# Kernel tuning notes

Hardware: AMD Instinct MI355X
Metric: run time of the kernel (lower is better)

Reference implementation:

```python
import jax, jax.numpy as jnp
import numpy as np

N = 50000       # nodes
E = 400000      # edges (before self-loops)
IN_C = 128
HID = 32        # hidden_channels per head
HEADS = 8
OUT_C = 64
K = 16          # num_clusters
NEG_SLOPE = 0.2
EPS = 1e-16


def setup_inputs() -> dict:
    key = jax.random.key(0)
    ks = jax.random.split(key, 14)
    g = lambda k, sh, sc: (jax.random.normal(k, sh, jnp.float32) * sc)
    return {
        "x": jax.random.normal(ks[0], (N, IN_C), jnp.float32),
        "edge_index": jax.random.randint(ks[1], (2, E), 0, N, dtype=jnp.int32),
        # GAT layer 1: in -> HEADS*HID
        "W1": g(ks[2], (IN_C, HEADS * HID), 0.08),
        "att_src1": g(ks[3], (HEADS, HID), 0.1),
        "att_dst1": g(ks[4], (HEADS, HID), 0.1),
        "b1": jnp.zeros((HEADS * HID,), jnp.float32),
        # GAT layer 2: HEADS*HID -> OUT_C, heads=1, concat=False
        "W2": g(ks[5], (HEADS * HID, OUT_C), 0.06),
        "att_src2": g(ks[6], (1, OUT_C), 0.1),
        "att_dst2": g(ks[7], (1, OUT_C), 0.1),
        "b2": jnp.zeros((OUT_C,), jnp.float32),
        # MLP head: OUT_C -> 128 -> K
        "Wm1": g(ks[8], (OUT_C, 128), 0.1),
        "bm1": jnp.zeros((128,), jnp.float32),
        "Wm2": g(ks[9], (128, K), 0.1),
        "bm2": jnp.zeros((K,), jnp.float32),
    }


def _gat_layer(x, W, att_src, att_dst, bias, src, dst, heads, ch, concat):
    # x: [N, F_in] -> h: [N, H, C]
    h = (x @ W).reshape(N, heads, ch)
    a_src = jnp.einsum('nhc,hc->nh', h, att_src)   # [N, H]
    a_dst = jnp.einsum('nhc,hc->nh', h, att_dst)   # [N, H]
    e = jax.nn.leaky_relu(a_src[src] + a_dst[dst], NEG_SLOPE)  # [Etot, H]
    # segment softmax over destination node
    m = jax.ops.segment_max(e, dst, num_segments=N)            # [N, H]
    ex = jnp.exp(e - m[dst])
    den = jax.ops.segment_sum(ex, dst, num_segments=N)         # [N, H]
    alpha = ex / (den[dst] + EPS)                              # [Etot, H]
    out = jax.ops.segment_sum(alpha[:, :, None] * h[src], dst, num_segments=N)  # [N, H, C]
    out = out.reshape(N, heads * ch) if concat else out.mean(axis=1)
    return out + bias


def reference(x, edge_index, W1, att_src1, att_dst1, b1, W2, att_src2, att_dst2, b2, Wm1, bm1, Wm2, bm2):
    # PyG GATConv adds self-loops by default
    loop = jnp.arange(N, dtype=edge_index.dtype)
    src = jnp.concatenate([edge_index[0], loop])
    dst = jnp.concatenate([edge_index[1], loop])
    # dropout layers are identity in eval mode
    h = jax.nn.elu(_gat_layer(x, W1, att_src1, att_dst1, b1, src, dst, HEADS, HID, True))
    embeddings = _gat_layer(h, W2, att_src2, att_dst2, b2, src, dst, 1, OUT_C, False)
    logits = jax.nn.relu(embeddings @ Wm1 + bm1) @ Wm2 + bm2
    s = jax.nn.softmax(logits, axis=1)
    return (s, embeddings)
```

## Files before the change

### kernel.cpp

```cpp
#include <hip/hip_runtime.h>
#include <hip/hip_fp16.h>
#include <math.h>

#define NNODES 50000
#define NEDGES 400000
#define INC    128
#define HC1    256
#define NHEADS 8
#define OUTC   64
#define NK     16
#define NEG_SLOPE 0.2f
#define EPS_F  1e-16f

typedef unsigned short u16;
typedef __attribute__((ext_vector_type(8))) short bf16x8;
typedef __attribute__((ext_vector_type(4))) float f32x4;

__device__ __forceinline__ float lrelu(float x){ return x > 0.f ? x : NEG_SLOPE * x; }
__device__ __forceinline__ float eluf(float x){ return x > 0.f ? x : (__expf(x) - 1.f); }
__device__ __forceinline__ float bf2f(u16 v){ return __uint_as_float((unsigned)v << 16); }
__device__ __forceinline__ u16 f2bf(float f){
    unsigned u = __float_as_uint(f);
    unsigned r = (u + 0x7FFFu + ((u >> 16) & 1u)) >> 16;
    return (u16)r;
}
__device__ __forceinline__ short f2bf_s(float f){ return (short)f2bf(f); }
__device__ __forceinline__ u16 f2h(float f){ return __half_as_ushort(__float2half(f)); }
__device__ __forceinline__ float h2f(u16 v){ return __half2float(__ushort_as_half(v)); }

__device__ __forceinline__ void fmix_lo(float& acc, unsigned w, float a){
    asm("v_fma_mix_f32 %0, %1, %2, %0 op_sel:[0,0,0] op_sel_hi:[1,0,0]"
        : "+v"(acc) : "v"(w), "v"(a));
}
__device__ __forceinline__ void fmix_hi(float& acc, unsigned w, float a){
    asm("v_fma_mix_f32 %0, %1, %2, %0 op_sel:[1,0,0] op_sel_hi:[1,0,0]"
        : "+v"(acc) : "v"(w), "v"(a));
}
__device__ __forceinline__ void mac8(float* acc, uint4 w, float a){
    fmix_lo(acc[0], w.x, a); fmix_hi(acc[1], w.x, a);
    fmix_lo(acc[2], w.y, a); fmix_hi(acc[3], w.y, a);
    fmix_lo(acc[4], w.z, a); fmix_hi(acc[5], w.z, a);
    fmix_lo(acc[6], w.w, a); fmix_hi(acc[7], w.w, a);
}
__device__ __forceinline__ void mac4(float4& acc, uint2 w, float a){
    fmix_lo(acc.x, w.x, a); fmix_hi(acc.y, w.x, a);
    fmix_lo(acc.z, w.y, a); fmix_hi(acc.w, w.y, a);
}

#define EB 1563
#define TB 232
__global__ void count_deg_tw_k(const int* __restrict__ dst, int* __restrict__ deg,
                               const float* __restrict__ W1, u16* __restrict__ W1t,
                               const float* __restrict__ W2, u16* __restrict__ W2t,
                               const float* __restrict__ Wm1, u16* __restrict__ W1mt,
                               const float* __restrict__ Wm2, u16* __restrict__ W2mt){
    if (blockIdx.x < EB){
        int e = blockIdx.x * 256 + threadIdx.x;
        if (e < NEDGES) atomicAdd(&deg[dst[e]], 1);
    } else {
        int i = (blockIdx.x - EB) * 256 + threadIdx.x;
        if (i < 32768){
            int n = i >> 7, k = i & 127;
            W1t[i] = f2bf(W1[k * 256 + n]);
        } else if (i < 49152){
            int ii = i - 32768;
            int n = ii >> 8, k = ii & 255;
            W2t[ii] = f2bf(W2[k * 64 + n]);
        } else if (i < 57344){
            int ii = i - 49152;
            int hd = ii >> 6, e = ii & 63;
            W1mt[ii] = f2bf(Wm1[e * 128 + hd]);
        } else if (i < 59392){
            int ii = i - 57344;
            int k = ii >> 7, hd = ii & 127;
            W2mt[ii] = f2bf(Wm2[hd * NK + k]);
        }
    }
}

__global__ void blocksum_k(const int* __restrict__ deg, int* __restrict__ bsum){
    __shared__ int sm[4];
    int i = blockIdx.x * 256 + threadIdx.x;
    int v = (i < NNODES) ? deg[i] : 0;
    for (int off = 1; off < 64; off <<= 1) v += __shfl_xor(v, off);
    int lane = threadIdx.x & 63, wid = threadIdx.x >> 6;
    if (lane == 0) sm[wid] = v;
    __syncthreads();
    if (threadIdx.x == 0) bsum[blockIdx.x] = sm[0] + sm[1] + sm[2] + sm[3];
}

__global__ void scan_write_k(const int* __restrict__ deg, const int* __restrict__ bsum,
                             int* __restrict__ rowptr){
    __shared__ int sm[4];
    __shared__ int sadd;
    int tid = threadIdx.x;
    int pv = (tid < blockIdx.x) ? bsum[tid] : 0;
    for (int off = 1; off < 64; off <<= 1) pv += __shfl_xor(pv, off);
    int lane = tid & 63, wid = tid >> 6;
    if (lane == 0) sm[wid] = pv;
    __syncthreads();
    if (tid == 0) sadd = sm[0] + sm[1] + sm[2] + sm[3];
    __syncthreads();

    int i = blockIdx.x * 256 + tid;
    int v = (i < NNODES) ? deg[i] : 0;
    int sv = v;
    for (int off = 1; off < 64; off <<= 1){ int t = __shfl_up(sv, off); if (lane >= off) sv += t; }
    __shared__ int wsum[4];
    if (lane == 63) wsum[wid] = sv;
    __syncthreads();
    int add = sadd;
    for (int w = 0; w < wid; w++) add += wsum[w];
    sv += add;
    if (i < NNODES) rowptr[i + 1] = sv;
    if (i == 0) rowptr[0] = 0;
}

__global__ void fill_csr_k(const int* __restrict__ src, const int* __restrict__ dst,
                           const int* __restrict__ rowptr, int* __restrict__ fillc,
                           int* __restrict__ col){
    int e = blockIdx.x * 256 + threadIdx.x;
    if (e < NEDGES){
        int d = dst[e];
        int pos = atomicAdd(&fillc[d], 1);
        col[rowptr[d] + pos] = src[e];
    }
}

__global__ __launch_bounds__(256, 4) void l1_k(const float* __restrict__ x, const u16* __restrict__ W1t,
                     const float* __restrict__ att_s, const float* __restrict__ att_d,
                     u16* __restrict__ h1bh, float* __restrict__ as1h, float* __restrict__ ad1h){
    __shared__ u16 Bs[16384];
    int tid = threadIdx.x;
    int lane = tid & 63, wid = tid >> 6;
    int ln = lane & 15, quad = lane >> 4;
    int m0 = blockIdx.x * 64 + wid * 16;
    int nb = blockIdx.y * 128;
    int hb = blockIdx.y * 4;
    int arow = m0 + ln; if (arow >= NNODES) arow = NNODES - 1;

#pragma unroll
    for (int it = 0; it < 8; it++){
        int p = it * 256 + tid;
        int c = p >> 6, l = p & 63;
        int snt = c & 7, skt = c >> 3;
        int sln = l & 15, sq = l >> 4;
        uint4 v = *(const uint4*)(W1t + (size_t)(nb + snt * 16 + sln) * INC + skt * 32 + sq * 8);
        *(uint4*)(&Bs[p * 8]) = v;
    }

    bf16x8 a[4];
#pragma unroll
    for (int kt = 0; kt < 4; kt++){
        const float* ap = x + (size_t)arow * INC + kt * 32 + quad * 8;
        float4 v0 = *(const float4*)ap;
        float4 v1 = *(const float4*)(ap + 4);
        bf16x8 t;
        t[0] = f2bf_s(v0.x); t[1] = f2bf_s(v0.y); t[2] = f2bf_s(v0.z); t[3] = f2bf_s(v0.w);
        t[4] = f2bf_s(v1.x); t[5] = f2bf_s(v1.y); t[6] = f2bf_s(v1.z); t[7] = f2bf_s(v1.w);
        a[kt] = t;
    }

    __syncthreads();

    f32x4 acc[8];
#pragma unroll
    for (int nt = 0; nt < 8; nt++) acc[nt] = (f32x4){0.f, 0.f, 0.f, 0.f};

#pragma unroll
    for (int kt = 0; kt < 4; kt++){
#pragma unroll
        for (int nt = 0; nt < 8; nt++){
            bf16x8 b = *(const bf16x8*)(&Bs[(kt * 8 + nt) * 512 + lane * 8]);
            acc[nt] = __builtin_amdgcn_mfma_f32_16x16x32_bf16(a[kt], b, acc[nt], 0, 0, 0);
        }
    }

#pragma unroll
    for (int i = 0; i < 4; i++){
        int r = m0 + quad * 4 + i;
        if (r < NNODES){
#pragma unroll
            for (int nt = 0; nt < 8; nt++){
                int c  = nb + nt * 16 + ln;
                int hh = c >> 5, c5 = c & 31;
                h1bh[((size_t)hh * NNODES + r) * 32 + c5] = f2h(acc[nt][i]);
            }
        }
    }

#pragma unroll
    for (int i = 0; i < 4; i++){
        int r = m0 + quad * 4 + i;
        float ps_keep = 0.f, pd_keep = 0.f;
#pragma unroll
        for (int h = 0; h < 4; h++){
            float ps = acc[2 * h][i]     * att_s[nb + h * 32 + ln]
                     + acc[2 * h + 1][i] * att_s[nb + h * 32 + 16 + ln];
            float pd = acc[2 * h][i]     * att_d[nb + h * 32 + ln]
                     + acc[2 * h + 1][i] * att_d[nb + h * 32 + 16 + ln];
            ps += __shfl_xor(ps, 1); pd += __shfl_xor(pd, 1);
            ps += __shfl_xor(ps, 2); pd += __shfl_xor(pd, 2);
            ps += __shfl_xor(ps, 4); pd += __shfl_xor(pd, 4);
            ps += __shfl_xor(ps, 8); pd += __shfl_xor(pd, 8);
            if (ln == h){ ps_keep = ps; pd_keep = pd; }
        }
        if (ln < 4 && r < NNODES){
            as1h[(size_t)(hb + ln) * NNODES + r] = ps_keep;
            ad1h[(size_t)(hb + ln) * NNODES + r] = pd_keep;
        }
    }
}

__global__ __launch_bounds__(256, 4) void l2_k(const u16* __restrict__ hL1b, const u16* __restrict__ W2t,
                     const float* __restrict__ att_s, const float* __restrict__ att_d,
                     u16* __restrict__ h2b, float* __restrict__ as2, float* __restrict__ ad2){
    __shared__ u16 Bs[16384];
    int tid = threadIdx.x;
    int lane = tid & 63, wid = tid >> 6;
    int ln = lane & 15, quad = lane >> 4;
    int m0 = blockIdx.x * 64 + wid * 16;
    int arow = m0 + ln; if (arow >= NNODES) arow = NNODES - 1;

#pragma unroll
    for (int it = 0; it < 8; it++){
        int p = it * 256 + tid;
        int c = p >> 6, l = p & 63;
        int snt = c & 3, skt = c >> 2;
        int sln = l & 15, sq = l >> 4;
        uint4 v = *(const uint4*)(W2t + (size_t)(snt * 16 + sln) * HC1 + skt * 32 + sq * 8);
        *(uint4*)(&Bs[p * 8]) = v;
    }

    __syncthreads();

    f32x4 acc[4];
#pragma unroll
    for (int nt = 0; nt < 4; nt++) acc[nt] = (f32x4){0.f, 0.f, 0.f, 0.f};

#pragma unroll
    for (int kt = 0; kt < 8; kt++){
        bf16x8 a = *(const bf16x8*)(hL1b + ((size_t)kt * NNODES + arow) * 32 + quad * 8);
#pragma unroll
        for (int nt = 0; nt < 4; nt++){
            bf16x8 b = *(const bf16x8*)(&Bs[(kt * 4 + nt) * 512 + lane * 8]);
            acc[nt] = __builtin_amdgcn_mfma_f32_16x16x32_bf16(a, b, acc[nt], 0, 0, 0);
        }
    }

#pragma unroll
    for (int i = 0; i < 4; i++){
        int r = m0 + quad * 4 + i;
        if (r < NNODES){
#pragma unroll
            for (int nt = 0; nt < 4; nt++)
                h2b[(size_t)r * OUTC + nt * 16 + ln] = f2h(acc[nt][i]);
        }
        float ps = acc[0][i] * att_s[ln]      + acc[1][i] * att_s[16 + ln]
                 + acc[2][i] * att_s[32 + ln] + acc[3][i] * att_s[48 + ln];
        float pd = acc[0][i] * att_d[ln]      + acc[1][i] * att_d[16 + ln]
                 + acc[2][i] * att_d[32 + ln] + acc[3][i] * att_d[48 + ln];
        ps += __shfl_xor(ps, 1); pd += __shfl_xor(pd, 1);
        ps += __shfl_xor(ps, 2); pd += __shfl_xor(pd, 2);
        ps += __shfl_xor(ps, 4); pd += __shfl_xor(pd, 4);
        ps += __shfl_xor(ps, 8); pd += __shfl_xor(pd, 8);
        if (ln == 0 && r < NNODES){ as2[r] = ps; ad2[r] = pd; }
    }
}

__global__ void gat1_agg_k(const u16* __restrict__ h1bh, const float* __restrict__ as1h,
                           const float* __restrict__ ad1h, const int* __restrict__ rowptr,
                           const int* __restrict__ col, const float* __restrict__ b1,
                           u16* __restrict__ outb){
    int lane = threadIdx.x & 63, wid = threadIdx.x >> 6;
    int g = lane >> 3, t = lane & 7;
    int h = blockIdx.x & 7;
    int d = (blockIdx.x >> 3) * 32 + wid * 8 + g;
    bool valid = (d < NNODES);
    int dd = valid ? d : (NNODES - 1);
    int row0 = rowptr[dd];
    int deg  = rowptr[dd + 1] - row0;

    const float* ash = as1h + (size_t)h * NNODES;
    float adst = ad1h[(size_t)h * NNODES + dd];
    const u16* hb = h1bh + (size_t)h * NNODES * 32;

    int sv0 = (t < deg)     ? col[row0 + t]     : dd;
    int sv1 = (8 + t < deg) ? col[row0 + 8 + t] : dd;
    uint2 wself = *(const uint2*)(hb + (size_t)dd * 32 + t * 4);
    float ev0 = ash[sv0];
    float ev1 = ash[sv1];

    float a_self = __expf(lrelu(ash[dd] + adst));
    float x0 = (t < deg)     ? __expf(lrelu(ev0 + adst)) : 0.f;
    float x1 = (8 + t < deg) ? __expf(lrelu(ev1 + adst)) : 0.f;

    float4 acc = make_float4(0.f, 0.f, 0.f, 0.f);
    mac4(acc, wself, a_self);

    int gb = g * 8;
    if (deg > 0){
        int s_arr[4]; float a_arr[4]; uint2 w_arr[4];
#pragma unroll
        for (int j = 0; j < 4; j++){ s_arr[j] = __shfl(sv0, gb + j); a_arr[j] = __shfl(x0, gb + j); }
#pragma unroll
        for (int j = 0; j < 4; j++) w_arr[j] = *(const uint2*)(hb + (size_t)s_arr[j] * 32 + t * 4);
#pragma unroll
        for (int j = 0; j < 4; j++) mac4(acc, w_arr[j], a_arr[j]);
        if (deg > 4){
#pragma unroll
            for (int j = 0; j < 4; j++){ s_arr[j] = __shfl(sv0, gb + 4 + j); a_arr[j] = __shfl(x0, gb + 4 + j); }
#pragma unroll
            for (int j = 0; j < 4; j++) w_arr[j] = *(const uint2*)(hb + (size_t)s_arr[j] * 32 + t * 4);
#pragma unroll
            for (int j = 0; j < 4; j++) mac4(acc, w_arr[j], a_arr[j]);
        }
    }
    if (deg > 8){
        int s_arr[4]; float a_arr[4]; uint2 w_arr[4];
#pragma unroll
        for (int j = 0; j < 4; j++){ s_arr[j] = __shfl(sv1, gb + j); a_arr[j] = __shfl(x1, gb + j); }
#pragma unroll
        for (int j = 0; j < 4; j++) w_arr[j] = *(const uint2*)(hb + (size_t)s_arr[j] * 32 + t * 4);
#pragma unroll
        for (int j = 0; j < 4; j++) mac4(acc, w_arr[j], a_arr[j]);
        if (deg > 12){
#pragma unroll
            for (int j = 0; j < 4; j++){ s_arr[j] = __shfl(sv1, gb + 4 + j); a_arr[j] = __shfl(x1, gb + 4 + j); }
#pragma unroll
            for (int j = 0; j < 4; j++) w_arr[j] = *(const uint2*)(hb + (size_t)s_arr[j] * 32 + t * 4);
#pragma unroll
            for (int j = 0; j < 4; j++) mac4(acc, w_arr[j], a_arr[j]);
        }
    }
    float tsum = 0.f;
    if (deg > 16){
        for (int idx = 16; idx < deg; idx++){
            int s = col[row0 + idx];
            float a = __expf(lrelu(ash[s] + adst));
            tsum += a;
            uint2 w = *(const uint2*)(hb + (size_t)s * 32 + t * 4);
            mac4(acc, w, a);
        }
    }

    float part = x0 + x1;
    part += __shfl_xor(part, 1);
    part += __shfl_xor(part, 2);
    part += __shfl_xor(part, 4);
    float rden = 1.f / (part + a_self + tsum + EPS_F);

    if (valid){
        float4 bb = *(const float4*)(b1 + h * 32 + t * 4);
        uint2 o;
        o.x = (unsigned)f2bf(eluf(acc.x * rden + bb.x)) | ((unsigned)f2bf(eluf(acc.y * rden + bb.y)) << 16);
        o.y = (unsigned)f2bf(eluf(acc.z * rden + bb.z)) | ((unsigned)f2bf(eluf(acc.w * rden + bb.w)) << 16);
        *(uint2*)(outb + ((size_t)h * NNODES + d) * 32 + t * 4) = o;
    }
}

__global__ void gat2_agg_k(const u16* __restrict__ h2b, const float* __restrict__ as2,
                           const float* __restrict__ ad2, const int* __restrict__ rowptr,
                           const int* __restrict__ col, const float* __restrict__ b2,
                           float* __restrict__ emb){
    int lane = threadIdx.x & 63, wid = threadIdx.x >> 6;
    int d = blockIdx.x * 4 + wid;
    int row0 = rowptr[d];
    int deg  = rowptr[d + 1] - row0;

    float adst = ad2[d];
    float a_self = __expf(lrelu(as2[d] + adst));

    if (deg <= 64){
        int sv = (lane < deg) ? col[row0 + lane] : d;
        float e_raw = as2[sv];

        int q = lane >> 4, c4 = (lane & 15) * 4;
        uint2 wself = *(const uint2*)(h2b + (unsigned)d * OUTC + c4);
        uint2 wpre[4];
#pragma unroll
        for (int k = 0; k < 4; k++){
            int s = __shfl(sv, k * 4 + q);
            wpre[k] = *(const uint2*)(h2b + (unsigned)s * OUTC + c4);
        }

        float x = (lane < deg) ? __expf(lrelu(e_raw + adst)) : 0.f;

        float a0 = (q == 0) ? a_self : 0.f;
        float4 acc = make_float4(0.f, 0.f, 0.f, 0.f);
        mac4(acc, wself, a0);
        {
            float a_arr[4];
#pragma unroll
            for (int k = 0; k < 4; k++) a_arr[k] = __shfl(x, k * 4 + q);
#pragma unroll
            for (int k = 0; k < 4; k++) mac4(acc, wpre[k], a_arr[k]);
        }
        for (int it0 = 16; it0 < deg; it0 += 16){
            int s_arr[4]; float a_arr[4];
#pragma unroll
            for (int k = 0; k < 4; k++){
                int itc = min(it0 + k * 4 + q, 63);
                s_arr[k] = __shfl(sv, itc);
                a_arr[k] = __shfl(x, itc);
            }
            uint2 w_arr[4];
#pragma unroll
            for (int k = 0; k < 4; k++)
                w_arr[k] = *(const uint2*)(h2b + (unsigned)s_arr[k] * OUTC + c4);
#pragma unroll
            for (int k = 0; k < 4; k++) mac4(acc, w_arr[k], a_arr[k]);
        }
        acc.x += __shfl_xor(acc.x, 16); acc.y += __shfl_xor(acc.y, 16);
        acc.z += __shfl_xor(acc.z, 16); acc.w += __shfl_xor(acc.w, 16);
        acc.x += __shfl_xor(acc.x, 32); acc.y += __shfl_xor(acc.y, 32);
        acc.z += __shfl_xor(acc.z, 32); acc.w += __shfl_xor(acc.w, 32);
        float vsum = x;
        for (int m = 1; m < 64; m <<= 1) vsum += __shfl_xor(vsum, m);
        float rden = 1.f / (vsum + a_self + EPS_F);
        if (lane < 16){
            float4 bb = *(const float4*)(b2 + c4);
            float4 o = make_float4(acc.x * rden + bb.x, acc.y * rden + bb.y,
                                   acc.z * rden + bb.z, acc.w * rden + bb.w);
            *(float4*)(emb + (size_t)d * OUTC + c4) = o;
        }
    } else {
        float vsum = a_self;
        float acc = a_self * h2f(h2b[(unsigned)d * OUTC + lane]);
        for (int idx = 0; idx < deg; idx++){
            int s = col[row0 + idx];
            float a = __expf(lrelu(as2[s] + adst));
            vsum += a;
            acc += a * h2f(h2b[(unsigned)s * OUTC + lane]);
        }
        emb[(size_t)d * OUTC + lane] = acc * (1.f / (vsum + EPS_F)) + b2[lane];
    }
}

__global__ void mlp_mfma_k(const float* __restrict__ emb, const u16* __restrict__ W1mt,
                           const float* __restrict__ bm1, const u16* __restrict__ W2mt,
                           const float* __restrict__ bm2, float* __restrict__ sout){
    __shared__ u16 hid[4][16][136];
    int lane = threadIdx.x & 63, wid = threadIdx.x >> 6;
    int ln = lane & 15, quad = lane >> 4;
    int m0 = blockIdx.x * 64 + wid * 16;
    int arow = m0 + ln; if (arow >= NNODES) arow = NNODES - 1;

    bf16x8 a[2];
#pragma unroll
    for (int kt = 0; kt < 2; kt++){
        const float* ap = emb + (size_t)arow * OUTC + kt * 32 + quad * 8;
        float4 v0 = *(const float4*)ap;
        float4 v1 = *(const float4*)(ap + 4);
        bf16x8 t;
        t[0] = f2bf_s(v0.x); t[1] = f2bf_s(v0.y); t[2] = f2bf_s(v0.z); t[3] = f2bf_s(v0.w);
        t[4] = f2bf_s(v1.x); t[5] = f2bf_s(v1.y); t[6] = f2bf_s(v1.z); t[7] = f2bf_s(v1.w);
        a[kt] = t;
    }

    f32x4 acc[8];
#pragma unroll
    for (int nt = 0; nt < 8; nt++) acc[nt] = (f32x4){0.f, 0.f, 0.f, 0.f};
#pragma unroll
    for (int kt = 0; kt < 2; kt++){
#pragma unroll
        for (int nt = 0; nt < 8; nt++){
            bf16x8 b = *(const bf16x8*)(W1mt + (size_t)(nt * 16 + ln) * OUTC + kt * 32 + quad * 8);
            acc[nt] = __builtin_amdgcn_mfma_f32_16x16x32_bf16(a[kt], b, acc[nt], 0, 0, 0);
        }
    }

#pragma unroll
    for (int nt = 0; nt < 8; nt++){
        float bb = bm1[nt * 16 + ln];
#pragma unroll
        for (int i = 0; i < 4; i++){
            float h = fmaxf(acc[nt][i] + bb, 0.f);
            hid[wid][quad * 4 + i][nt * 16 + ln] = f2bf(h);
        }
    }

    f32x4 acc2 = (f32x4){0.f, 0.f, 0.f, 0.f};
#pragma unroll
    for (int kt = 0; kt < 4; kt++){
        bf16x8 ah = *(const bf16x8*)&hid[wid][ln][kt * 32 + quad * 8];
        bf16x8 bw = *(const bf16x8*)(W2mt + (size_t)ln * 128 + kt * 32 + quad * 8);
        acc2 = __builtin_amdgcn_mfma_f32_16x16x32_bf16(ah, bw, acc2, 0, 0, 0);
    }

    float bcl = bm2[ln];
#pragma unroll
    for (int i = 0; i < 4; i++){
        int r = m0 + quad * 4 + i;
        float lg = acc2[i] + bcl;
        float m = lg;
        m = fmaxf(m, __shfl_xor(m, 1));
        m = fmaxf(m, __shfl_xor(m, 2));
        m = fmaxf(m, __shfl_xor(m, 4));
        m = fmaxf(m, __shfl_xor(m, 8));
        float ex = __expf(lg - m);
        float s = ex;
        s += __shfl_xor(s, 1);
        s += __shfl_xor(s, 2);
        s += __shfl_xor(s, 4);
        s += __shfl_xor(s, 8);
        if (r < NNODES) sout[(size_t)r * NK + ln] = ex / s;
    }
}

extern "C" void kernel_launch(void* const* d_in, const int* in_sizes, int n_in,
                              void* d_out, int out_size, void* d_ws, size_t ws_size,
                              hipStream_t stream){
    const float* x      = (const float*)d_in[0];
    const int*   ei     = (const int*)d_in[1];
    const int*   srcv   = ei;
    const int*   dstv   = ei + NEDGES;
    const float* W1     = (const float*)d_in[2];
    const float* att_s1 = (const float*)d_in[3];
    const float* att_d1 = (const float*)d_in[4];
    const float* b1     = (const float*)d_in[5];
    const float* W2     = (const float*)d_in[6];
    const float* att_s2 = (const float*)d_in[7];
    const float* att_d2 = (const float*)d_in[8];
    const float* b2     = (const float*)d_in[9];
    const float* Wm1    = (const float*)d_in[10];
    const float* bm1    = (const float*)d_in[11];
    const float* Wm2    = (const float*)d_in[12];
    const float* bm2    = (const float*)d_in[13];

    float* out     = (float*)d_out;
    float* emb_out = out + (size_t)NNODES * NK;

    u16* h1b   = (u16*)d_ws;
    u16* hL1b  = h1b  + (size_t)NNODES * HC1;
    u16* h2b   = hL1b + (size_t)NNODES * HC1;
    u16* W1t   = h2b  + (size_t)NNODES * OUTC;
    u16* W2t   = W1t + 256 * 128;
    u16* W1mt  = W2t + 64 * 256;
    u16* W2mt  = W1mt + 128 * 64;
    float* as1 = (float*)(W2mt + 16 * 128);
    float* ad1 = as1 + (size_t)NNODES * NHEADS;
    float* as2 = ad1 + (size_t)NNODES * NHEADS;
    float* ad2 = as2 + NNODES;
    int* deg    = (int*)(ad2 + NNODES);
    int* fillc  = deg + NNODES;
    int* rowptr = fillc + NNODES;
    int* bsum   = rowptr + NNODES + 1;
    int* colv   = bsum + 256;

    hipMemsetAsync(deg, 0, 2 * NNODES * sizeof(int), stream);

    const int NB = (NNODES + 255) / 256;

    count_deg_tw_k<<<EB + TB, 256, 0, stream>>>(dstv, deg, W1, W1t, W2, W2t, Wm1, W1mt, Wm2, W2mt);
    blocksum_k<<<NB, 256, 0, stream>>>(deg, bsum);
    scan_write_k<<<NB, 256, 0, stream>>>(deg, bsum, rowptr);
    fill_csr_k<<<(NEDGES + 255) / 256, 256, 0, stream>>>(srcv, dstv, rowptr, fillc, colv);

    const int MB = (NNODES + 63) / 64;

    l1_k<<<dim3(MB, 2), 256, 0, stream>>>(x, W1t, att_s1, att_d1, h1b, as1, ad1);
    gat1_agg_k<<<8 * ((NNODES + 31) / 32), 256, 0, stream>>>(h1b, as1, ad1, rowptr, colv, b1, hL1b);

    l2_k<<<MB, 256, 0, stream>>>(hL1b, W2t, att_s2, att_d2, h2b, as2, ad2);
    gat2_agg_k<<<NNODES / 4, 256, 0, stream>>>(h2b, as2, ad2, rowptr, colv, b2, emb_out);

    mlp_mfma_k<<<MB, 256, 0, stream>>>(emb_out, W1mt, bm1, W2mt, bm2, out);
}
```

Baseline: 252.4 us.

## Remap GAT layer-1 aggregation to 16 lanes per node with parallel neighbour teams

Each destination node in the layer-1 aggregation is now served by 16 lanes arranged as four teams of four. Each team gathers a different neighbour's 32-channel bf16 row with 16-byte loads instead of 8-byte loads. Partial sums across teams are combined with cross-lane shuffles before the ELU and bf16 store. The aim is more memory-level parallelism on the irregular gathers and fewer serial edge steps per node, at the cost of extra shuffle reductions and twice as many blocks.

```diff
diff --git a/kernel.cpp b/kernel.cpp
--- a/kernel.cpp
+++ b/kernel.cpp
@@ -273,89 +273,78 @@
                            const int* __restrict__ col, const float* __restrict__ b1,
                            u16* __restrict__ outb){
     int lane = threadIdx.x & 63, wid = threadIdx.x >> 6;
-    int g = lane >> 3, t = lane & 7;
+    int l16 = lane & 15;
+    int grp = (lane >> 4) & 3;
+    int team = l16 >> 2;
+    int tql  = l16 & 3;
+    int base16 = lane & 48;
+
     int h = blockIdx.x & 7;
-    int d = (blockIdx.x >> 3) * 32 + wid * 8 + g;
-    bool valid = (d < NNODES);
-    int dd = valid ? d : (NNODES - 1);
-    int row0 = rowptr[dd];
-    int deg  = rowptr[dd + 1] - row0;
+    int d = (blockIdx.x >> 3) * 16 + wid * 4 + grp;
+
+    int row0 = rowptr[d];
+    int deg  = rowptr[d + 1] - row0;
 
     const float* ash = as1h + (size_t)h * NNODES;
-    float adst = ad1h[(size_t)h * NNODES + dd];
+    float adst = ad1h[(size_t)h * NNODES + d];
     const u16* hb = h1bh + (size_t)h * NNODES * 32;
 
-    int sv0 = (t < deg)     ? col[row0 + t]     : dd;
-    int sv1 = (8 + t < deg) ? col[row0 + 8 + t] : dd;
-    uint2 wself = *(const uint2*)(hb + (size_t)dd * 32 + t * 4);
-    float ev0 = ash[sv0];
-    float ev1 = ash[sv1];
-
-    float a_self = __expf(lrelu(ash[dd] + adst));
-    float x0 = (t < deg)     ? __expf(lrelu(ev0 + adst)) : 0.f;
-    float x1 = (8 + t < deg) ? __expf(lrelu(ev1 + adst)) : 0.f;
-
-    float4 acc = make_float4(0.f, 0.f, 0.f, 0.f);
-    mac4(acc, wself, a_self);
-
-    int gb = g * 8;
-    if (deg > 0){
-        int s_arr[4]; float a_arr[4]; uint2 w_arr[4];
-#pragma unroll
-        for (int j = 0; j < 4; j++){ s_arr[j] = __shfl(sv0, gb + j); a_arr[j] = __shfl(x0, gb + j); }
-#pragma unroll
-        for (int j = 0; j < 4; j++) w_arr[j] = *(const uint2*)(hb + (size_t)s_arr[j] * 32 + t * 4);
-#pragma unroll
-        for (int j = 0; j < 4; j++) mac4(acc, w_arr[j], a_arr[j]);
-        if (deg > 4){
-#pragma unroll
-            for (int j = 0; j < 4; j++){ s_arr[j] = __shfl(sv0, gb + 4 + j); a_arr[j] = __shfl(x0, gb + 4 + j); }
-#pragma unroll
-            for (int j = 0; j < 4; j++) w_arr[j] = *(const uint2*)(hb + (size_t)s_arr[j] * 32 + t * 4);
-#pragma unroll
-            for (int j = 0; j < 4; j++) mac4(acc, w_arr[j], a_arr[j]);
-        }
-    }
-    if (deg > 8){
-        int s_arr[4]; float a_arr[4]; uint2 w_arr[4];
-#pragma unroll
-        for (int j = 0; j < 4; j++){ s_arr[j] = __shfl(sv1, gb + j); a_arr[j] = __shfl(x1, gb + j); }
-#pragma unroll
-        for (int j = 0; j < 4; j++) w_arr[j] = *(const uint2*)(hb + (size_t)s_arr[j] * 32 + t * 4);
-#pragma unroll
-        for (int j = 0; j < 4; j++) mac4(acc, w_arr[j], a_arr[j]);
-        if (deg > 12){
-#pragma unroll
-            for (int j = 0; j < 4; j++){ s_arr[j] = __shfl(sv1, gb + 4 + j); a_arr[j] = __shfl(x1, gb + 4 + j); }
-#pragma unroll
-            for (int j = 0; j < 4; j++) w_arr[j] = *(const uint2*)(hb + (size_t)s_arr[j] * 32 + t * 4);
-#pragma unroll
-            for (int j = 0; j < 4; j++) mac4(acc, w_arr[j], a_arr[j]);
-        }
-    }
+    int sv = (l16 < deg) ? col[row0 + l16] : d;
+
+    int s_arr[4];
+#pragma unroll
+    for (int k = 0; k < 4; k++) s_arr[k] = __shfl(sv, base16 + 4 * k + team);
+    uint4 w_arr[4];
+#pragma unroll
+    for (int k = 0; k < 4; k++)
+        w_arr[k] = *(const uint4*)(hb + (size_t)s_arr[k] * 32 + tql * 8);
+    uint4 wself = *(const uint4*)(hb + (size_t)d * 32 + tql * 8);
+    float ev = ash[sv];
+    float a_self = __expf(lrelu(ash[d] + adst));
+
+    float xv = (l16 < deg) ? __expf(lrelu(ev + adst)) : 0.f;
+
+    float acc[8] = {0.f, 0.f, 0.f, 0.f, 0.f, 0.f, 0.f, 0.f};
+    mac8(acc, wself, (team == 0) ? a_self : 0.f);
+#pragma unroll
+    for (int k = 0; k < 4; k++){
+        float a = __shfl(xv, base16 + 4 * k + team);
+        mac8(acc, w_arr[k], a);
+    }
+
     float tsum = 0.f;
-    if (deg > 16){
-        for (int idx = 16; idx < deg; idx++){
-            int s = col[row0 + idx];
-            float a = __expf(lrelu(ash[s] + adst));
-            tsum += a;
-            uint2 w = *(const uint2*)(hb + (size_t)s * 32 + t * 4);
-            mac4(acc, w, a);
-        }
-    }
-
-    float part = x0 + x1;
+    for (int idx = 16; idx < deg; idx += 4){
+        int e = idx + team;
+        int cj = (e < deg) ? col[row0 + e] : d;
+        float a = (e < deg) ? __expf(lrelu(ash[cj] + adst)) : 0.f;
+        uint4 w = *(const uint4*)(hb + (size_t)cj * 32 + tql * 8);
+        mac8(acc, w, a);
+        if (tql == 0) tsum += a;
+    }
+
+    float part = xv + tsum;
     part += __shfl_xor(part, 1);
     part += __shfl_xor(part, 2);
     part += __shfl_xor(part, 4);
-    float rden = 1.f / (part + a_self + tsum + EPS_F);
-
-    if (valid){
-        float4 bb = *(const float4*)(b1 + h * 32 + t * 4);
-        uint2 o;
-        o.x = (unsigned)f2bf(eluf(acc.x * rden + bb.x)) | ((unsigned)f2bf(eluf(acc.y * rden + bb.y)) << 16);
-        o.y = (unsigned)f2bf(eluf(acc.z * rden + bb.z)) | ((unsigned)f2bf(eluf(acc.w * rden + bb.w)) << 16);
-        *(uint2*)(outb + ((size_t)h * NNODES + d) * 32 + t * 4) = o;
+    part += __shfl_xor(part, 8);
+    float rden = 1.f / (part + a_self + EPS_F);
+
+#pragma unroll
+    for (int k = 0; k < 8; k++){
+        acc[k] += __shfl_xor(acc[k], 4);
+        acc[k] += __shfl_xor(acc[k], 8);
+    }
+
+    if (team == 0){
+        const float* bp = b1 + h * 32 + tql * 8;
+        float4 b0 = *(const float4*)bp;
+        float4 b4 = *(const float4*)(bp + 4);
+        uint4 o;
+        o.x = (unsigned)f2bf(eluf(acc[0] * rden + b0.x)) | ((unsigned)f2bf(eluf(acc[1] * rden + b0.y)) << 16);
+        o.y = (unsigned)f2bf(eluf(acc[2] * rden + b0.z)) | ((unsigned)f2bf(eluf(acc[3] * rden + b0.w)) << 16);
+        o.z = (unsigned)f2bf(eluf(acc[4] * rden + b4.x)) | ((unsigned)f2bf(eluf(acc[5] * rden + b4.y)) << 16);
+        o.w = (unsigned)f2bf(eluf(acc[6] * rden + b4.z)) | ((unsigned)f2bf(eluf(acc[7] * rden + b4.w)) << 16);
+        *(uint4*)(outb + ((size_t)h * NNODES + d) * 32 + tql * 8) = o;
     }
 }
 
@@ -560,7 +549,7 @@
     const int MB = (NNODES + 63) / 64;
 
     l1_k<<<dim3(MB, 2), 256, 0, stream>>>(x, W1t, att_s1, att_d1, h1b, as1, ad1);
-    gat1_agg_k<<<8 * ((NNODES + 31) / 32), 256, 0, stream>>>(h1b, as1, ad1, rowptr, colv, b1, hL1b);
+    gat1_agg_k<<<8 * (NNODES / 16), 256, 0, stream>>>(h1b, as1, ad1, rowptr, colv, b1, hL1b);
 
     l2_k<<<MB, 256, 0, stream>>>(hL1b, W2t, att_s2, att_d2, h2b, as2, ad2);
     gat2_agg_k<<<NNODES / 4, 256, 0, stream>>>(h2b, as2, ad2, rowptr, colv, b2, emb_out);
```

After: 256.8 us. No clear change (+1.7%).

## Slice layer-2 features into 8-channel planes and split aggregation per slice

Applied to the files above, without the earlier changes.

Layer-2 features now go out in a sliced layout, one plane per 8 channels (one 16-byte row per node in each plane). The aggregation kernel gives each 16-lane group one destination node and one channel slice, so blocks working on the same slice gather from a compact 800 KB plane with 16-byte loads, which should improve cache locality. The exponentials and column indices are now recomputed once per slice (8x redundancy), and the old high-degree fallback is gone in favour of a strided loop. Grid size changes to 8 slices times node groups.

```diff
diff --git a/kernel.cpp b/kernel.cpp
--- a/kernel.cpp
+++ b/kernel.cpp
@@ -214,7 +214,7 @@
 
 __global__ __launch_bounds__(256, 4) void l2_k(const u16* __restrict__ hL1b, const u16* __restrict__ W2t,
                      const float* __restrict__ att_s, const float* __restrict__ att_d,
-                     u16* __restrict__ h2b, float* __restrict__ as2, float* __restrict__ ad2){
+                     u16* __restrict__ h2bs, float* __restrict__ as2, float* __restrict__ ad2){
     __shared__ u16 Bs[16384];
     int tid = threadIdx.x;
     int lane = tid & 63, wid = tid >> 6;
@@ -253,8 +253,11 @@
         int r = m0 + quad * 4 + i;
         if (r < NNODES){
 #pragma unroll
-            for (int nt = 0; nt < 4; nt++)
-                h2b[(size_t)r * OUTC + nt * 16 + ln] = f2h(acc[nt][i]);
+            for (int nt = 0; nt < 4; nt++){
+                int c  = nt * 16 + ln;
+                int sl = c >> 3, pos = c & 7;
+                h2bs[((size_t)sl * NNODES + r) * 8 + pos] = f2h(acc[nt][i]);
+            }
         }
         float ps = acc[0][i] * att_s[ln]      + acc[1][i] * att_s[16 + ln]
                  + acc[2][i] * att_s[32 + ln] + acc[3][i] * att_s[48 + ln];
@@ -359,81 +362,65 @@
     }
 }
 
-__global__ void gat2_agg_k(const u16* __restrict__ h2b, const float* __restrict__ as2,
+__global__ void gat2_agg_k(const u16* __restrict__ h2bs, const float* __restrict__ as2,
                            const float* __restrict__ ad2, const int* __restrict__ rowptr,
                            const int* __restrict__ col, const float* __restrict__ b2,
                            float* __restrict__ emb){
     int lane = threadIdx.x & 63, wid = threadIdx.x >> 6;
-    int d = blockIdx.x * 4 + wid;
+    int l16 = lane & 15;
+    int grp = (lane >> 4) & 3;
+    int s = blockIdx.x & 7;
+    int d = (blockIdx.x >> 3) * 16 + wid * 4 + grp;
+
     int row0 = rowptr[d];
     int deg  = rowptr[d + 1] - row0;
 
     float adst = ad2[d];
     float a_self = __expf(lrelu(as2[d] + adst));
-
-    if (deg <= 64){
-        int sv = (lane < deg) ? col[row0 + lane] : d;
-        float e_raw = as2[sv];
-
-        int q = lane >> 4, c4 = (lane & 15) * 4;
-        uint2 wself = *(const uint2*)(h2b + (unsigned)d * OUTC + c4);
-        uint2 wpre[4];
-#pragma unroll
-        for (int k = 0; k < 4; k++){
-            int s = __shfl(sv, k * 4 + q);
-            wpre[k] = *(const uint2*)(h2b + (unsigned)s * OUTC + c4);
-        }
-
-        float x = (lane < deg) ? __expf(lrelu(e_raw + adst)) : 0.f;
-
-        float a0 = (q == 0) ? a_self : 0.f;
-        float4 acc = make_float4(0.f, 0.f, 0.f, 0.f);
-        mac4(acc, wself, a0);
-        {
-            float a_arr[4];
-#pragma unroll
-            for (int k = 0; k < 4; k++) a_arr[k] = __shfl(x, k * 4 + q);
-#pragma unroll
-            for (int k = 0; k < 4; k++) mac4(acc, wpre[k], a_arr[k]);
-        }
-        for (int it0 = 16; it0 < deg; it0 += 16){
-            int s_arr[4]; float a_arr[4];
-#pragma unroll
-            for (int k = 0; k < 4; k++){
-                int itc = min(it0 + k * 4 + q, 63);
-                s_arr[k] = __shfl(sv, itc);
-                a_arr[k] = __shfl(x, itc);
-            }
-            uint2 w_arr[4];
-#pragma unroll
-            for (int k = 0; k < 4; k++)
-                w_arr[k] = *(const uint2*)(h2b + (unsigned)s_arr[k] * OUTC + c4);
-#pragma unroll
-            for (int k = 0; k < 4; k++) mac4(acc, w_arr[k], a_arr[k]);
-        }
-        acc.x += __shfl_xor(acc.x, 16); acc.y += __shfl_xor(acc.y, 16);
-        acc.z += __shfl_xor(acc.z, 16); acc.w += __shfl_xor(acc.w, 16);
-        acc.x += __shfl_xor(acc.x, 32); acc.y += __shfl_xor(acc.y, 32);
-        acc.z += __shfl_xor(acc.z, 32); acc.w += __shfl_xor(acc.w, 32);
-        float vsum = x;
-        for (int m = 1; m < 64; m <<= 1) vsum += __shfl_xor(vsum, m);
-        float rden = 1.f / (vsum + a_self + EPS_F);
-        if (lane < 16){
-            float4 bb = *(const float4*)(b2 + c4);
-            float4 o = make_float4(acc.x * rden + bb.x, acc.y * rden + bb.y,
-                                   acc.z * rden + bb.z, acc.w * rden + bb.w);
-            *(float4*)(emb + (size_t)d * OUTC + c4) = o;
-        }
-    } else {
-        float vsum = a_self;
-        float acc = a_self * h2f(h2b[(unsigned)d * OUTC + lane]);
-        for (int idx = 0; idx < deg; idx++){
-            int s = col[row0 + idx];
-            float a = __expf(lrelu(as2[s] + adst));
-            vsum += a;
-            acc += a * h2f(h2b[(unsigned)s * OUTC + lane]);
-        }
-        emb[(size_t)d * OUTC + lane] = acc * (1.f / (vsum + EPS_F)) + b2[lane];
+    const u16* hs = h2bs + (size_t)s * NNODES * 8;
+
+    int sv = (l16 < deg) ? col[row0 + l16] : d;
+    float er = as2[sv];
+    uint4 w = *(const uint4*)(hs + (size_t)sv * 8);
+    float x = (l16 < deg) ? __expf(lrelu(er + adst)) : 0.f;
+
+    float acc[8] = {0.f, 0.f, 0.f, 0.f, 0.f, 0.f, 0.f, 0.f};
+    mac8(acc, w, x);
+    if (l16 == 0){
+        uint4 ws = *(const uint4*)(hs + (size_t)d * 8);
+        mac8(acc, ws, a_self);
+    }
+    float xsum = x;
+    for (int idx = 16 + l16; idx < deg; idx += 16){
+        int cj = col[row0 + idx];
+        float a = __expf(lrelu(as2[cj] + adst));
+        uint4 wt = *(const uint4*)(hs + (size_t)cj * 8);
+        mac8(acc, wt, a);
+        xsum += a;
+    }
+
+#pragma unroll
+    for (int k = 0; k < 8; k++){
+        acc[k] += __shfl_xor(acc[k], 1);
+        acc[k] += __shfl_xor(acc[k], 2);
+        acc[k] += __shfl_xor(acc[k], 4);
+        acc[k] += __shfl_xor(acc[k], 8);
+    }
+    xsum += __shfl_xor(xsum, 1);
+    xsum += __shfl_xor(xsum, 2);
+    xsum += __shfl_xor(xsum, 4);
+    xsum += __shfl_xor(xsum, 8);
+    float rden = 1.f / (xsum + a_self + EPS_F);
+
+    if (l16 == 0){
+        const float* bp = b2 + s * 8;
+        float4 o0 = make_float4(acc[0] * rden + bp[0], acc[1] * rden + bp[1],
+                                acc[2] * rden + bp[2], acc[3] * rden + bp[3]);
+        float4 o1 = make_float4(acc[4] * rden + bp[4], acc[5] * rden + bp[5],
+                                acc[6] * rden + bp[6], acc[7] * rden + bp[7]);
+        float* op = emb + (size_t)d * OUTC + s * 8;
+        *(float4*)op = o0;
+        *(float4*)(op + 4) = o1;
     }
 }
 
@@ -563,7 +550,7 @@
     gat1_agg_k<<<8 * ((NNODES + 31) / 32), 256, 0, stream>>>(h1b, as1, ad1, rowptr, colv, b1, hL1b);
 
     l2_k<<<MB, 256, 0, stream>>>(hL1b, W2t, att_s2, att_d2, h2b, as2, ad2);
-    gat2_agg_k<<<NNODES / 4, 256, 0, stream>>>(h2b, as2, ad2, rowptr, colv, b2, emb_out);
+    gat2_agg_k<<<8 * (NNODES / 16), 256, 0, stream>>>(h2b, as2, ad2, rowptr, colv, b2, emb_out);
 
     mlp_mfma_k<<<MB, 256, 0, stream>>>(emb_out, W1mt, bm1, W2mt, bm2, out);
 }
```

Result: slower. 273.2 us (+8.2%).
